# Optimization experiments

Hardware: AMD Instinct MI355X
Metric: run time of the kernel (lower is better)

## Reference

```python
import jax, jax.numpy as jnp
import numpy as np

STRIDE = 16
NUM_A = 9
POS_TH, NEG_TH = 0.7, 0.3
FG, BG, IGN = 1.0, 0.0, 2.0
CAP = 128  # BATCH_SIZE * 0.5 for both fg and bg


def _generate_base_anchors(base_size=16, ratios=(0.5, 1.0, 2.0), scales=(8, 16, 32)):
    w = h = float(base_size)
    xc = yc = 0.5 * (base_size - 1)
    size = w * h
    out = []
    for r in ratios:
        ws = np.round(np.sqrt(size / r))
        hs = np.round(ws * r)
        for s in scales:
            W, H = ws * s, hs * s
            out.append([xc - 0.5 * (W - 1), yc - 0.5 * (H - 1),
                        xc + 0.5 * (W - 1), yc + 0.5 * (H - 1)])
    return np.asarray(out, dtype=np.float32)  # [9,4]


def _all_anchors(H, W):
    base = _generate_base_anchors()
    sx = np.arange(W, dtype=np.float32) * STRIDE
    sy = np.arange(H, dtype=np.float32) * STRIDE
    xs, ys = np.meshgrid(sx, sy)  # row-major over (h, w)
    shifts = np.stack([xs.ravel(), ys.ravel(), xs.ravel(), ys.ravel()], 1)
    return jnp.asarray((shifts[:, None, :] + base[None, :, :]).reshape(-1, 4))  # [H*W*9,4], order (h,w,a)


def _forward(scores, gt, im_w, im_h):
    H, W = scores.shape[2], scores.shape[3]
    anchors = _all_anchors(H, W)  # [N,4]
    valid = (anchors[:, 0] >= 0.) & (anchors[:, 1] >= 0.) & \
            (anchors[:, 2] < im_w) & (anchors[:, 3] < im_h)
    # pairwise IoU with +1 box convention
    aw = anchors[:, 2] - anchors[:, 0] + 1.
    ah = anchors[:, 3] - anchors[:, 1] + 1.
    a_area = jnp.where((aw > 0) & (ah > 0), aw * ah, 0.)
    gw = gt[:, 2] - gt[:, 0] + 1.
    gh = gt[:, 3] - gt[:, 1] + 1.
    g_area = jnp.where((gw > 0) & (gh > 0), gw * gh, 0.)
    ix1 = jnp.maximum(anchors[:, None, 0], gt[None, :, 0])
    iy1 = jnp.maximum(anchors[:, None, 1], gt[None, :, 1])
    ix2 = jnp.minimum(anchors[:, None, 2], gt[None, :, 2])
    iy2 = jnp.minimum(anchors[:, None, 3], gt[None, :, 3])
    iw = ix2 - ix1 + 1.
    ih = iy2 - iy1 + 1.
    inter = jnp.where((iw > 0) & (ih > 0), iw * ih, 0.)
    ovl = inter / (a_area[:, None] + g_area[None, :] - inter)  # [N,G]
    ovl_m = jnp.where(valid[:, None], ovl, -1.)  # exclude invalid anchors
    a_argmax = jnp.argmax(ovl, axis=1)           # best gt per anchor
    a_max = jnp.max(ovl, axis=1)
    g_max = jnp.max(ovl_m, axis=0)               # best (valid) anchor overlap per gt
    gt_fg = jnp.any(ovl_m == g_max[None, :], axis=1) & valid
    labels = jnp.where(valid & (a_max < NEG_TH), BG, IGN)
    labels = jnp.where(gt_fg, FG, labels)
    labels = jnp.where(valid & (a_max >= POS_TH), FG, labels)
    # random subsample fg/bg down to CAP each (matches npr.choice semantics in distribution)
    kf, kb = jax.random.split(jax.random.key(42))
    def subsample(lbl, mask, k):
        s = jnp.where(mask, jax.random.uniform(k, lbl.shape), jnp.inf)
        ranks = jnp.argsort(jnp.argsort(s))
        keep = ranks < jnp.minimum(jnp.sum(mask), CAP)
        return jnp.where(mask & ~keep, IGN, lbl)
    labels = subsample(labels, labels == FG, kf)
    labels = subsample(labels, labels == BG, kb)
    num_ni = jnp.sum(labels != IGN).astype(jnp.float32)
    gts = gt[a_argmax]
    ax = (anchors[:, 2] + anchors[:, 0]) * 0.5
    ay = (anchors[:, 3] + anchors[:, 1]) * 0.5
    gwm = gts[:, 2] - gts[:, 0] + 1.
    ghm = gts[:, 3] - gts[:, 1] + 1.
    gx = (gts[:, 2] + gts[:, 0]) * 0.5
    gy = (gts[:, 3] + gts[:, 1]) * 0.5
    adj = jnp.stack([(gx - ax) / aw, (gy - ay) / ah,
                     jnp.log(gwm / aw), jnp.log(ghm / ah)], axis=1)  # [N,4]
    adj = jnp.where(valid[:, None], adj, 0.)
    wts = jnp.where((labels == FG)[:, None], 1.0 / num_ni, 0.) * jnp.ones((1, 4), jnp.float32)
    labels_out = labels.reshape(1, H, W, NUM_A).transpose(0, 3, 1, 2) \
                       .reshape(1, 1, NUM_A * H, W).astype(jnp.int32)
    adj_out = adj.reshape(1, H, W, 4 * NUM_A).transpose(0, 3, 1, 2)
    wts_out = wts.reshape(1, H, W, 4 * NUM_A).transpose(0, 3, 1, 2)
    return labels_out, adj_out, wts_out


def setup_inputs() -> dict:
    key = jax.random.key(0)
    k1, k2, k3 = jax.random.split(key, 3)
    scores = jax.random.normal(k1, (1, 18, 256, 256), dtype=jnp.float32)
    G = 64
    cxy = jax.random.uniform(k2, (G, 2), minval=100., maxval=3900.)
    wh = jax.random.uniform(k3, (G, 2), minval=32., maxval=512.)
    x1y1 = jnp.clip(cxy - wh * 0.5, 0., 4095.)
    x2y2 = jnp.clip(cxy + wh * 0.5, 0., 4095.)
    gt = jnp.concatenate([x1y1, x2y2], axis=1)  # [G,4] = x1,y1,x2,y2
    return {"anchor_object_scores": scores, "ground_truth_boxes": gt,
            "im_w": 4096, "im_h": 4096}


def reference(anchor_object_scores, ground_truth_boxes, im_w, im_h):
    return _forward(anchor_object_scores, ground_truth_boxes, im_w, im_h)
```

## Files before the change

### kernel.cpp

```cpp
#include <hip/hip_runtime.h>
#include <stdint.h>


#define NUM_A 9
#define HW 65536
#define N_ANCH 589824
#define NG 64
#define CAPK 128u
#define NBIN 2048
#define BIN_SHIFT 12
#define CAND_CAP 4096

#define LAB_BG 0u
#define LAB_FG 1u
#define LAB_IGN 2u

#define OFF_GMAX8 0
#define OFF_HF    512
#define OFF_HB    (OFF_HF + NBIN)
#define OFF_CNTF  (OFF_HF + 2*NBIN)
#define OFF_CNTB  (OFF_CNTF + 1)
#define OFF_DONE2 (OFF_CNTF + 2)
#define OFF_SEL   (OFF_CNTF + 4)
#define OFF_CANDF 4620
#define OFF_CANDB (OFF_CANDF + 2*CAND_CAP)
#define OFF_LABM  (OFF_CANDB + 2*CAND_CAP)
#define ZERO_BEG  OFF_HF
#define ZERO_END  OFF_CANDF
#define NZ        (ZERO_END - ZERO_BEG)

__constant__ float BA[NUM_A][4] = {
  { -84.f,  -40.f,  99.f,  55.f}, {-176.f,  -88.f, 191.f, 103.f},
  {-360.f, -184.f, 375.f, 199.f}, { -56.f,  -56.f,  71.f,  71.f},
  {-120.f, -120.f, 135.f, 135.f}, {-248.f, -248.f, 263.f, 263.f},
  { -36.f,  -80.f,  51.f,  95.f}, { -80.f, -168.f,  95.f, 183.f},
  {-168.f, -344.f, 183.f, 359.f}};

__host__ __device__ static inline void tf2x32(uint32_t k0, uint32_t k1,
                                              uint32_t x0, uint32_t x1,
                                              uint32_t* o0, uint32_t* o1) {
  const uint32_t ks2 = k0 ^ k1 ^ 0x1BD11BDAu;
#define TF_R(r) { x0 += x1; x1 = (x1 << (r)) | (x1 >> (32 - (r))); x1 ^= x0; }
  x0 += k0; x1 += k1;
  TF_R(13) TF_R(15) TF_R(26) TF_R(6)
  x0 += k1;  x1 += ks2 + 1u;
  TF_R(17) TF_R(29) TF_R(16) TF_R(24)
  x0 += ks2; x1 += k0 + 2u;
  TF_R(13) TF_R(15) TF_R(26) TF_R(6)
  x0 += k0;  x1 += k1 + 3u;
  TF_R(17) TF_R(29) TF_R(16) TF_R(24)
  x0 += k1;  x1 += ks2 + 4u;
  TF_R(13) TF_R(15) TF_R(26) TF_R(6)
  x0 += ks2; x1 += k0 + 5u;
#undef TF_R
  *o0 = x0; *o1 = x1;
}

__device__ static inline uint32_t mant_of(uint32_t k0, uint32_t k1, uint32_t n) {
  uint32_t o0, o1;
  tf2x32(k0, k1, 0u, n, &o0, &o1);
  return (o0 ^ o1) >> 9;
}

__device__ static inline float iou1(float a0, float a1, float a2, float a3,
                                    float aarea, float g0, float g1, float g2,
                                    float g3, float garea) {
  #pragma clang fp contract(off)
  float ix1 = fmaxf(a0, g0);
  float iy1 = fmaxf(a1, g1);
  float ix2 = fminf(a2, g2);
  float iy2 = fminf(a3, g3);
  float iw = ix2 - ix1 + 1.0f;
  float ih = iy2 - iy1 + 1.0f;
  float inter = (iw > 0.0f && ih > 0.0f) ? iw * ih : 0.0f;
  float den = aarea + garea - inter;
  return inter / den;
}

__global__ __launch_bounds__(256) void k_gmax(const float* __restrict__ gt,
                                              const int* __restrict__ imw_p,
                                              const int* __restrict__ imh_p,
                                              uint32_t* __restrict__ ws) {
  #pragma clang fp contract(off)
  int tid = threadIdx.x;
  int b = blockIdx.x;
  int gid = b * 256 + tid;
  if (gid < NZ) ws[ZERO_BEG + gid] = 0u;

  int g = b >> 3, sl = b & 7;
  float g0 = gt[g*4+0], g1 = gt[g*4+1], g2 = gt[g*4+2], g3 = gt[g*4+3];
  float gw = g2 - g0 + 1.0f, gh = g3 - g1 + 1.0f;
  float ga = (gw > 0.0f && gh > 0.0f) ? gw * gh : 0.0f;
  float imw = (float)imw_p[0], imh = (float)imh_p[0];

  float mx = 0.0f;
  for (int a = 0; a < NUM_A; a++) {
    float b0 = BA[a][0], b1 = BA[a][1], b2 = BA[a][2], b3 = BA[a][3];
    int wlo = max(0,   (int)floorf((g0 - 1.0f - b2) * 0.0625f));
    int whi = min(255, (int)ceilf ((g2 + 1.0f - b0) * 0.0625f));
    int hlo = max(0,   (int)floorf((g1 - 1.0f - b3) * 0.0625f));
    int hhi = min(255, (int)ceilf ((g3 + 1.0f - b1) * 0.0625f));
    int wx = whi - wlo + 1, wy = hhi - hlo + 1;
    if (wx <= 0 || wy <= 0) continue;
    int tot = wx * wy;
    for (int idx = sl * 256 + tid; idx < tot; idx += 2048) {
      int h = hlo + idx / wx, w = wlo + idx % wx;
      float sx = (float)(w << 4), sy = (float)(h << 4);
      float x1 = b0 + sx, y1 = b1 + sy, x2 = b2 + sx, y2 = b3 + sy;
      float aw = x2 - x1 + 1.0f, ah = y2 - y1 + 1.0f;
      float aarea = aw * ah;
      bool vld = (x1 >= 0.0f) && (y1 >= 0.0f) && (x2 < imw) && (y2 < imh);
      float o = iou1(x1, y1, x2, y2, aarea, g0, g1, g2, g3, ga);
      if (vld) mx = fmaxf(mx, o);
    }
  }
  #pragma unroll
  for (int s = 32; s >= 1; s >>= 1) mx = fmaxf(mx, __shfl_xor(mx, s, 64));
  __shared__ float wmax[4];
  if ((tid & 63) == 0) wmax[tid >> 6] = mx;
  __syncthreads();
  if (tid == 0) {
    float m = fmaxf(fmaxf(wmax[0], wmax[1]), fmaxf(wmax[2], wmax[3]));
    ws[OFF_GMAX8 + g * 8 + sl] = __float_as_uint(m);
  }
}

__global__ __launch_bounds__(256) void k_main(const float* __restrict__ gt,
                                              const int* __restrict__ imw_p,
                                              const int* __restrict__ imh_p,
                                              float* __restrict__ out_adj,
                                              uint32_t* __restrict__ ws,
                                              uint32_t kf0, uint32_t kf1,
                                              uint32_t kb0, uint32_t kb1) {
  #pragma clang fp contract(off)
  __shared__ float sg0[NG], sg1[NG], sg2[NG], sg3[NG], sga[NG], sgm[NG];
  __shared__ uint32_t sh[2 * NBIN];
  __shared__ unsigned long long sMask[4];
  __shared__ int sAnyZero, sLast;
  int tid = threadIdx.x;
  {
    uint4* sh4 = (uint4*)sh;
    #pragma unroll
    for (int k = 0; k < 4; k++) sh4[tid + k * 256] = make_uint4(0, 0, 0, 0);
  }
  if (tid == 0) sAnyZero = 0;
  if (tid < NG) {
    const float4 g4 = ((const float4*)gt)[tid];
    sg0[tid] = g4.x; sg1[tid] = g4.y; sg2[tid] = g4.z; sg3[tid] = g4.w;
    float gw = g4.z - g4.x + 1.0f, gh = g4.w - g4.y + 1.0f;
    sga[tid] = (gw > 0.0f && gh > 0.0f) ? gw * gh : 0.0f;
    uint32_t mm = 0u;
    #pragma unroll
    for (int j = 0; j < 8; j++) mm = max(mm, ws[OFF_GMAX8 + tid * 8 + j]);
    sgm[tid] = __uint_as_float(mm);
    if (mm == 0u) atomicOr(&sAnyZero, 1);
  }
  __syncthreads();

  int b = blockIdx.x;
  int a = b >> 6, hb = (b & 63) << 2;
  float BA0 = BA[a][0], BA1 = BA[a][1], BA2 = BA[a][2], BA3 = BA[a][3];

  {
    int wv = tid >> 6, g = tid & 63;
    float sy = (float)((hb + wv) << 4);
    float ihp = fminf(BA3 + sy, sg3[g]) - fmaxf(BA1 + sy, sg1[g]) + 1.0f;
    unsigned long long mk = __ballot(ihp > 0.0f);
    if (g == 0) sMask[wv] = mk;
  }
  __syncthreads();

  float imw = (float)imw_p[0], imh = (float)imh_p[0];
  int w = tid;
  float sx = (float)(w << 4);
  float A0 = BA0 + sx, A2 = BA2 + sx;
  float aw = A2 - A0 + 1.0f;
  float A1v[4], A3v[4];
  #pragma unroll
  for (int r = 0; r < 4; r++) {
    float sy = (float)((hb + r) << 4);
    A1v[r] = BA1 + sy; A3v[r] = BA3 + sy;
  }
  float ah = A3v[0] - A1v[0] + 1.0f;
  float aarea = aw * ah;
  bool xv = (A0 >= 0.0f) && (A2 < imw);

  unsigned long long mk0 = sMask[0], mk1 = sMask[1],
                     mk2 = sMask[2], mk3 = sMask[3];
  unsigned long long uni = mk0 | mk1 | mk2 | mk3;
  float amaxv[4] = {0.f, 0.f, 0.f, 0.f};
  int bgv[4] = {0, 0, 0, 0};
  uint32_t afv = 0u;
  while (uni) {
    int g = __ffsll(uni) - 1;
    uni &= uni - 1;
    float iw = fminf(A2, sg2[g]) - fmaxf(A0, sg0[g]) + 1.0f;
    if (!__any(iw > 0.0f)) continue;
    if (iw > 0.0f) {
      float base = aarea + sga[g];
      float gy1 = sg1[g], gy2 = sg3[g], gm = sgm[g];
#define DO_ROW(r, mk)                                                     \
      if ((mk >> g) & 1ull) {                                             \
        float ih = fminf(A3v[r], gy2) - fmaxf(A1v[r], gy1) + 1.0f;        \
        float inter = iw * ih;                                            \
        float o = inter / (base - inter);                                 \
        if (o > amaxv[r]) { amaxv[r] = o; bgv[r] = g; }                   \
        if (o == gm) afv |= (1u << r);                                    \
      }
      DO_ROW(0, mk0) DO_ROW(1, mk1) DO_ROW(2, mk2) DO_ROW(3, mk3)
#undef DO_ROW
    }
  }

  bool anyZ = (sAnyZero != 0);
  #pragma unroll
  for (int r = 0; r < 4; r++) {
    int hw = (hb + r) * 256 + w;
    bool valid = xv && (A1v[r] >= 0.0f) && (A3v[r] < imh);
    float amax = amaxv[r];
    bool anyfg = (((afv >> r) & 1u) || anyZ) && valid;
    uint32_t lab;
    if (!valid)                       lab = LAB_IGN;
    else if (anyfg || amax >= 0.7f)   lab = LAB_FG;
    else if (amax < 0.3f)             lab = LAB_BG;
    else                              lab = LAB_IGN;

    float adj0 = 0.f, adj1 = 0.f, adj2 = 0.f, adj3 = 0.f;
    if (valid) {
      int bg = bgv[r];
      float G0 = sg0[bg], G1 = sg1[bg], G2 = sg2[bg], G3 = sg3[bg];
      float ax = (A2 + A0) * 0.5f, ay = (A3v[r] + A1v[r]) * 0.5f;
      float gwm = G2 - G0 + 1.0f, ghm = G3 - G1 + 1.0f;
      float gx = (G2 + G0) * 0.5f, gy = (G3 + G1) * 0.5f;
      adj0 = (gx - ax) / aw;
      adj1 = (gy - ay) / ah;
      adj2 = logf(gwm / aw);
      adj3 = logf(ghm / ah);
    }
    int c4 = a * 4;
    out_adj[(c4 + 0) * HW + hw] = adj0;
    out_adj[(c4 + 1) * HW + hw] = adj1;
    out_adj[(c4 + 2) * HW + hw] = adj2;
    out_adj[(c4 + 3) * HW + hw] = adj3;

    uint32_t m = 0u;
    uint32_t n = (uint32_t)(hw * 9 + a);
    if (lab != LAB_IGN) {
      uint32_t kk0 = (lab == LAB_FG) ? kf0 : kb0;
      uint32_t kk1 = (lab == LAB_FG) ? kf1 : kb1;
      m = mant_of(kk0, kk1, n);
      atomicAdd(&sh[((lab == LAB_FG) ? 0 : NBIN) + (m >> BIN_SHIFT)], 1u);
    }
    ws[OFF_LABM + a * HW + hw] = (lab << 24) | m;
  }

  __syncthreads();
  for (int i = tid; i < 2 * NBIN; i += 256) {
    uint32_t v = sh[i];
    if (v) atomicAdd(&ws[OFF_HF + i], v);
  }
  __syncthreads();
  if (tid == 0)
    sLast = (atomicAdd(&ws[OFF_DONE2], 1u) == 575u) ? 1 : 0;
  __syncthreads();
  if (sLast) {
    for (int cls = 0; cls < 2; cls++) {
      uint32_t* hist = ws + (cls ? OFF_HB : OFF_HF);
      uint32_t* sel = ws + OFF_SEL + cls * 4;
      uint32_t loc[8], s = 0;
      #pragma unroll
      for (int j = 0; j < 8; j++) {
        loc[j] = __hip_atomic_load(&hist[tid * 8 + j], __ATOMIC_RELAXED,
                                   __HIP_MEMORY_SCOPE_AGENT);
        s += loc[j];
      }
      sh[tid] = s; __syncthreads();
      for (int off = 1; off < 256; off <<= 1) {
        uint32_t v = (tid >= off) ? sh[tid - off] : 0u;
        __syncthreads();
        sh[tid] += v;
        __syncthreads();
      }
      uint32_t total = sh[255];
      uint32_t K = total < CAPK ? total : CAPK;
      if (tid == 0) {
        sel[3] = K;
        if (K == 0u) { sel[0] = 0xFFFFFFFFu; sel[1] = 0u; sel[2] = 0u; }
      }
      if (K > 0u) {
        uint32_t myC = sh[tid], pvC = (tid == 0) ? 0u : sh[tid - 1];
        if (myC >= K && pvC < K) {
          uint32_t cum = pvC; int bb = tid * 8;
          for (int j = 0; j < 8; j++) {
            if (cum + loc[j] >= K) { bb = tid * 8 + j; break; }
            cum += loc[j];
          }
          sel[0] = (uint32_t)bb; sel[1] = cum; sel[2] = K - cum;
        }
      }
      __syncthreads();
    }
  }
}

__global__ __launch_bounds__(256) void k_emit(float* __restrict__ out_lab,
                                              float* __restrict__ out_wts,
                                              uint32_t* __restrict__ ws) {
  int t = blockIdx.x * 256 + threadIdx.x;
  uint32_t lm = ws[OFF_LABM + t];
  uint32_t lab = lm >> 24;
  uint32_t m = lm & 0x7FFFFFu;
  uint32_t Kf = ws[OFF_SEL + 3], Kb = ws[OFF_SEL + 7];
  float inv = 1.0f / (float)(Kf + Kb);
  int a = t >> 16, hw = t & 65535;
  uint32_t n = (uint32_t)(hw * 9 + a);

  float outv = 2.0f, wv = 0.0f;
  if (lab == LAB_FG) {
    uint32_t b = m >> BIN_SHIFT, bf = ws[OFF_SEL + 0];
    if (b < bf) { outv = 1.0f; wv = inv; }
    else if (b == bf) {
      uint32_t idx = atomicAdd(&ws[OFF_CNTF], 1u);
      if (idx < CAND_CAP)
        ((uint64_t*)(ws + OFF_CANDF))[idx] = ((uint64_t)m << 20) | (uint64_t)n;
    }
  } else if (lab == LAB_BG) {
    uint32_t b = m >> BIN_SHIFT, bb = ws[OFF_SEL + 4];
    if (b < bb) { outv = 0.0f; }
    else if (b == bb) {
      uint32_t idx = atomicAdd(&ws[OFF_CNTB], 1u);
      if (idx < CAND_CAP)
        ((uint64_t*)(ws + OFF_CANDB))[idx] = ((uint64_t)m << 20) | (uint64_t)n;
    }
  }
  out_lab[t] = outv;
  int c4 = a * 4;
  out_wts[(c4 + 0) * HW + hw] = wv;
  out_wts[(c4 + 1) * HW + hw] = wv;
  out_wts[(c4 + 2) * HW + hw] = wv;
  out_wts[(c4 + 3) * HW + hw] = wv;
}

__global__ __launch_bounds__(256) void k_fixup(float* __restrict__ out_lab,
                                               float* __restrict__ out_wts,
                                               uint32_t* __restrict__ ws) {
  __shared__ uint64_t sc[CAND_CAP];
  int cls = blockIdx.x;
  uint32_t cnt = ws[cls == 0 ? OFF_CNTF : OFF_CNTB];
  uint32_t C = cnt < CAND_CAP ? cnt : CAND_CAP;
  uint32_t need = ws[OFF_SEL + cls * 4 + 2];
  uint32_t Kf = ws[OFF_SEL + 3], Kb = ws[OFF_SEL + 7];
  float inv = 1.0f / (float)(Kf + Kb);
  const uint64_t* cand =
      (const uint64_t*)(ws + (cls == 0 ? OFF_CANDF : OFF_CANDB));
  for (uint32_t i = threadIdx.x; i < C; i += 256) sc[i] = cand[i];
  __syncthreads();
  for (uint32_t i = threadIdx.x; i < C; i += 256) {
    uint64_t k = sc[i];
    uint32_t r = 0;
    for (uint32_t j = 0; j < C; j++) r += (sc[j] < k) ? 1u : 0u;
    if (r < need) {
      uint32_t n = (uint32_t)(k & 0xFFFFFu);
      uint32_t a = n % 9u, hw = n / 9u;
      uint32_t t = a * HW + hw;
      if (cls == 0) {
        out_lab[t] = 1.0f;
        #pragma unroll
        for (int j = 0; j < 4; j++) out_wts[(a * 4 + j) * HW + hw] = inv;
      } else {
        out_lab[t] = 0.0f;
      }
    }
  }
}

extern "C" void kernel_launch(void* const* d_in, const int* in_sizes, int n_in,
                              void* d_out, int out_size, void* d_ws,
                              size_t ws_size, hipStream_t stream) {
  const float* gt  = (const float*)d_in[1];
  const int*   imw = (const int*)d_in[2];
  const int*   imh = (const int*)d_in[3];
  float* out      = (float*)d_out;
  float* out_lab  = out;
  float* out_adj  = out + N_ANCH;
  float* out_wts  = out + 5 * N_ANCH;
  uint32_t* ws = (uint32_t*)d_ws;

  uint32_t kf0, kf1, kb0, kb1;
  tf2x32(0u, 42u, 0u, 0u, &kf0, &kf1);
  tf2x32(0u, 42u, 0u, 1u, &kb0, &kb1);

  hipLaunchKernelGGL(k_gmax, dim3(NG * 8), dim3(256), 0, stream, gt, imw, imh,
                     ws);
  hipLaunchKernelGGL(k_main, dim3(576), dim3(256), 0, stream, gt, imw, imh,
                     out_adj, ws, kf0, kf1, kb0, kb1);
  hipLaunchKernelGGL(k_emit, dim3(N_ANCH / 256), dim3(256), 0, stream, out_lab,
                     out_wts, ws);
  hipLaunchKernelGGL(k_fixup, dim3(2), dim3(256), 0, stream, out_lab, out_wts,
                     ws);
}
```

Measured before the change: 101.9 us.

## Fuse four kernels into one cooperative kernel with grid syncs

Merges the gt-max, main IoU/label, emit and fixup kernels into a single cooperative launch of 576 blocks separated by grid-wide barriers. Labels and random mantissas are kept in registers across the barrier instead of being written to and reread from workspace. The gt-max phase is spread over all 576 blocks (9 per gt) instead of 512. This removes three kernel launch gaps and a workspace round trip, but adds grid-sync costs and depends on all 576 blocks being co-resident. If the cooperative launch fails, it falls back to the old four-kernel path.

```diff
diff --git a/kernel.cpp b/kernel.cpp
--- a/kernel.cpp
+++ b/kernel.cpp
@@ -1,5 +1,8 @@
 #include <hip/hip_runtime.h>
+#include <hip/hip_cooperative_groups.h>
 #include <stdint.h>
+
+namespace cg = cooperative_groups;
 
 
 #define NUM_A 9
@@ -14,6 +17,18 @@
 #define LAB_BG 0u
 #define LAB_FG 1u
 #define LAB_IGN 2u
+
+#define F_OFF_GMAX 0
+#define F_OFF_HF   1024
+#define F_OFF_HB   (F_OFF_HF + NBIN)
+#define F_OFF_CNTF (F_OFF_HF + 2*NBIN)
+#define F_OFF_CNTB (F_OFF_CNTF + 1)
+#define F_OFF_DONE (F_OFF_CNTF + 2)
+#define F_OFF_SEL  (F_OFF_CNTF + 4)
+#define F_OFF_CANDF 5132
+#define F_OFF_CANDB (F_OFF_CANDF + 2*CAND_CAP)
+#define F_ZERO_BEG F_OFF_HF
+#define F_NZ (F_OFF_CANDF - F_OFF_HF)
 
 #define OFF_GMAX8 0
 #define OFF_HF    512
@@ -77,73 +92,81 @@
   return inter / den;
 }
 
-__global__ __launch_bounds__(256) void k_gmax(const float* __restrict__ gt,
-                                              const int* __restrict__ imw_p,
-                                              const int* __restrict__ imh_p,
-                                              uint32_t* __restrict__ ws) {
+__global__ __launch_bounds__(256, 3) void k_fused(
+    const float* __restrict__ gt, const int* __restrict__ imw_p,
+    const int* __restrict__ imh_p, float* __restrict__ out_lab,
+    float* __restrict__ out_adj, float* __restrict__ out_wts,
+    uint32_t* __restrict__ ws, uint32_t kf0, uint32_t kf1, uint32_t kb0,
+    uint32_t kb1) {
   #pragma clang fp contract(off)
+  cg::grid_group grd = cg::this_grid();
+
+  __shared__ uint64_t SMEM[CAND_CAP];
+  uint32_t* SW = (uint32_t*)SMEM;
+  float* sg0 = (float*)(SW + 0);
+  float* sg1 = (float*)(SW + 64);
+  float* sg2 = (float*)(SW + 128);
+  float* sg3 = (float*)(SW + 192);
+  float* sga = (float*)(SW + 256);
+  float* sgm = (float*)(SW + 320);
+  uint32_t* sh = SW + 384;
+  unsigned long long* sMask = (unsigned long long*)(SW + 4480);
+  int* sAnyZero = (int*)(SW + 4488);
+  int* sLast = (int*)(SW + 4489);
+  float* wmax = (float*)(SW + 4490);
+
   int tid = threadIdx.x;
   int b = blockIdx.x;
-  int gid = b * 256 + tid;
-  if (gid < NZ) ws[ZERO_BEG + gid] = 0u;
-
-  int g = b >> 3, sl = b & 7;
-  float g0 = gt[g*4+0], g1 = gt[g*4+1], g2 = gt[g*4+2], g3 = gt[g*4+3];
-  float gw = g2 - g0 + 1.0f, gh = g3 - g1 + 1.0f;
-  float ga = (gw > 0.0f && gh > 0.0f) ? gw * gh : 0.0f;
-  float imw = (float)imw_p[0], imh = (float)imh_p[0];
-
-  float mx = 0.0f;
-  for (int a = 0; a < NUM_A; a++) {
-    float b0 = BA[a][0], b1 = BA[a][1], b2 = BA[a][2], b3 = BA[a][3];
-    int wlo = max(0,   (int)floorf((g0 - 1.0f - b2) * 0.0625f));
-    int whi = min(255, (int)ceilf ((g2 + 1.0f - b0) * 0.0625f));
-    int hlo = max(0,   (int)floorf((g1 - 1.0f - b3) * 0.0625f));
-    int hhi = min(255, (int)ceilf ((g3 + 1.0f - b1) * 0.0625f));
-    int wx = whi - wlo + 1, wy = hhi - hlo + 1;
-    if (wx <= 0 || wy <= 0) continue;
-    int tot = wx * wy;
-    for (int idx = sl * 256 + tid; idx < tot; idx += 2048) {
-      int h = hlo + idx / wx, w = wlo + idx % wx;
-      float sx = (float)(w << 4), sy = (float)(h << 4);
-      float x1 = b0 + sx, y1 = b1 + sy, x2 = b2 + sx, y2 = b3 + sy;
-      float aw = x2 - x1 + 1.0f, ah = y2 - y1 + 1.0f;
-      float aarea = aw * ah;
-      bool vld = (x1 >= 0.0f) && (y1 >= 0.0f) && (x2 < imw) && (y2 < imh);
-      float o = iou1(x1, y1, x2, y2, aarea, g0, g1, g2, g3, ga);
-      if (vld) mx = fmaxf(mx, o);
-    }
-  }
-  #pragma unroll
-  for (int s = 32; s >= 1; s >>= 1) mx = fmaxf(mx, __shfl_xor(mx, s, 64));
-  __shared__ float wmax[4];
-  if ((tid & 63) == 0) wmax[tid >> 6] = mx;
-  __syncthreads();
-  if (tid == 0) {
-    float m = fmaxf(fmaxf(wmax[0], wmax[1]), fmaxf(wmax[2], wmax[3]));
-    ws[OFF_GMAX8 + g * 8 + sl] = __float_as_uint(m);
-  }
-}
-
-__global__ __launch_bounds__(256) void k_main(const float* __restrict__ gt,
-                                              const int* __restrict__ imw_p,
-                                              const int* __restrict__ imh_p,
-                                              float* __restrict__ out_adj,
-                                              uint32_t* __restrict__ ws,
-                                              uint32_t kf0, uint32_t kf1,
-                                              uint32_t kb0, uint32_t kb1) {
-  #pragma clang fp contract(off)
-  __shared__ float sg0[NG], sg1[NG], sg2[NG], sg3[NG], sga[NG], sgm[NG];
-  __shared__ uint32_t sh[2 * NBIN];
-  __shared__ unsigned long long sMask[4];
-  __shared__ int sAnyZero, sLast;
-  int tid = threadIdx.x;
+
+  {
+    int gid = b * 256 + tid;
+    if (gid < F_NZ) ws[F_ZERO_BEG + gid] = 0u;
+
+    int g = b / 9, sl = b - g * 9;
+    float g0 = gt[g*4+0], g1 = gt[g*4+1], g2 = gt[g*4+2], g3 = gt[g*4+3];
+    float gw = g2 - g0 + 1.0f, gh = g3 - g1 + 1.0f;
+    float ga = (gw > 0.0f && gh > 0.0f) ? gw * gh : 0.0f;
+    float imw = (float)imw_p[0], imh = (float)imh_p[0];
+
+    float mx = 0.0f;
+    for (int aa = 0; aa < NUM_A; aa++) {
+      float b0 = BA[aa][0], b1 = BA[aa][1], b2 = BA[aa][2], b3 = BA[aa][3];
+      int wlo = max(0,   (int)floorf((g0 - 1.0f - b2) * 0.0625f));
+      int whi = min(255, (int)ceilf ((g2 + 1.0f - b0) * 0.0625f));
+      int hlo = max(0,   (int)floorf((g1 - 1.0f - b3) * 0.0625f));
+      int hhi = min(255, (int)ceilf ((g3 + 1.0f - b1) * 0.0625f));
+      int wx = whi - wlo + 1, wy = hhi - hlo + 1;
+      if (wx <= 0 || wy <= 0) continue;
+      int tot = wx * wy;
+      for (int idx = sl * 256 + tid; idx < tot; idx += 2304) {
+        int h = hlo + idx / wx, w2 = wlo + idx % wx;
+        float sx = (float)(w2 << 4), sy = (float)(h << 4);
+        float x1 = b0 + sx, y1 = b1 + sy, x2 = b2 + sx, y2 = b3 + sy;
+        float aw = x2 - x1 + 1.0f, ah = y2 - y1 + 1.0f;
+        float aarea = aw * ah;
+        bool vld = (x1 >= 0.0f) && (y1 >= 0.0f) && (x2 < imw) && (y2 < imh);
+        float o = iou1(x1, y1, x2, y2, aarea, g0, g1, g2, g3, ga);
+        if (vld) mx = fmaxf(mx, o);
+      }
+    }
+    #pragma unroll
+    for (int s = 32; s >= 1; s >>= 1) mx = fmaxf(mx, __shfl_xor(mx, s, 64));
+    if ((tid & 63) == 0) wmax[tid >> 6] = mx;
+    __syncthreads();
+    if (tid == 0) {
+      float m = fmaxf(fmaxf(wmax[0], wmax[1]), fmaxf(wmax[2], wmax[3]));
+      ws[F_OFF_GMAX + g * 16 + sl] = __float_as_uint(m);
+    }
+  }
+
+  grd.sync();
+
   {
     uint4* sh4 = (uint4*)sh;
     #pragma unroll
     for (int k = 0; k < 4; k++) sh4[tid + k * 256] = make_uint4(0, 0, 0, 0);
   }
-  if (tid == 0) sAnyZero = 0;
+  if (tid == 0) *sAnyZero = 0;
   if (tid < NG) {
     const float4 g4 = ((const float4*)gt)[tid];
     sg0[tid] = g4.x; sg1[tid] = g4.y; sg2[tid] = g4.z; sg3[tid] = g4.w;
@@ -151,13 +174,15 @@
     sga[tid] = (gw > 0.0f && gh > 0.0f) ? gw * gh : 0.0f;
     uint32_t mm = 0u;
     #pragma unroll
-    for (int j = 0; j < 8; j++) mm = max(mm, ws[OFF_GMAX8 + tid * 8 + j]);
+    for (int j = 0; j < 9; j++)
+      mm = max(mm, __hip_atomic_load(&ws[F_OFF_GMAX + tid * 16 + j],
+                                     __ATOMIC_RELAXED,
+                                     __HIP_MEMORY_SCOPE_AGENT));
     sgm[tid] = __uint_as_float(mm);
-    if (mm == 0u) atomicOr(&sAnyZero, 1);
-  }
-  __syncthreads();
-
-  int b = blockIdx.x;
+    if (mm == 0u) atomicOr(sAnyZero, 1);
+  }
+  __syncthreads();
+
   int a = b >> 6, hb = (b & 63) << 2;
   float BA0 = BA[a][0], BA1 = BA[a][1], BA2 = BA[a][2], BA3 = BA[a][3];
 
@@ -212,6 +237,315 @@
     }
   }
 
+  bool anyZ = (*sAnyZero != 0);
+  uint32_t lm[4];
+  #pragma unroll
+  for (int r = 0; r < 4; r++) {
+    int hw = (hb + r) * 256 + w;
+    bool valid = xv && (A1v[r] >= 0.0f) && (A3v[r] < imh);
+    float amax = amaxv[r];
+    bool anyfg = (((afv >> r) & 1u) || anyZ) && valid;
+    uint32_t lab;
+    if (!valid)                       lab = LAB_IGN;
+    else if (anyfg || amax >= 0.7f)   lab = LAB_FG;
+    else if (amax < 0.3f)             lab = LAB_BG;
+    else                              lab = LAB_IGN;
+
+    float adj0 = 0.f, adj1 = 0.f, adj2 = 0.f, adj3 = 0.f;
+    if (valid) {
+      int bg = bgv[r];
+      float G0 = sg0[bg], G1 = sg1[bg], G2 = sg2[bg], G3 = sg3[bg];
+      float ax = (A2 + A0) * 0.5f, ay = (A3v[r] + A1v[r]) * 0.5f;
+      float gwm = G2 - G0 + 1.0f, ghm = G3 - G1 + 1.0f;
+      float gx = (G2 + G0) * 0.5f, gy = (G3 + G1) * 0.5f;
+      adj0 = (gx - ax) / aw;
+      adj1 = (gy - ay) / ah;
+      adj2 = logf(gwm / aw);
+      adj3 = logf(ghm / ah);
+    }
+    int c4 = a * 4;
+    out_adj[(c4 + 0) * HW + hw] = adj0;
+    out_adj[(c4 + 1) * HW + hw] = adj1;
+    out_adj[(c4 + 2) * HW + hw] = adj2;
+    out_adj[(c4 + 3) * HW + hw] = adj3;
+
+    uint32_t m = 0u;
+    uint32_t n = (uint32_t)(hw * 9 + a);
+    if (lab != LAB_IGN) {
+      uint32_t kk0 = (lab == LAB_FG) ? kf0 : kb0;
+      uint32_t kk1 = (lab == LAB_FG) ? kf1 : kb1;
+      m = mant_of(kk0, kk1, n);
+      atomicAdd(&sh[((lab == LAB_FG) ? 0 : NBIN) + (m >> BIN_SHIFT)], 1u);
+    }
+    lm[r] = (lab << 24) | m;
+  }
+
+  __syncthreads();
+  for (int i = tid; i < 2 * NBIN; i += 256) {
+    uint32_t v = sh[i];
+    if (v) atomicAdd(&ws[F_OFF_HF + i], v);
+  }
+  __syncthreads();
+  if (tid == 0)
+    *sLast = (atomicAdd(&ws[F_OFF_DONE], 1u) == 575u) ? 1 : 0;
+  __syncthreads();
+  if (*sLast) {
+    for (int cls = 0; cls < 2; cls++) {
+      uint32_t* hist = ws + (cls ? F_OFF_HB : F_OFF_HF);
+      uint32_t* sel = ws + F_OFF_SEL + cls * 4;
+      uint32_t loc[8], s = 0;
+      #pragma unroll
+      for (int j = 0; j < 8; j++) {
+        loc[j] = __hip_atomic_load(&hist[tid * 8 + j], __ATOMIC_RELAXED,
+                                   __HIP_MEMORY_SCOPE_AGENT);
+        s += loc[j];
+      }
+      sh[tid] = s; __syncthreads();
+      for (int off = 1; off < 256; off <<= 1) {
+        uint32_t v = (tid >= off) ? sh[tid - off] : 0u;
+        __syncthreads();
+        sh[tid] += v;
+        __syncthreads();
+      }
+      uint32_t total = sh[255];
+      uint32_t K = total < CAPK ? total : CAPK;
+      if (tid == 0) {
+        sel[3] = K;
+        if (K == 0u) { sel[0] = 0xFFFFFFFFu; sel[1] = 0u; sel[2] = 0u; }
+      }
+      if (K > 0u) {
+        uint32_t myC = sh[tid], pvC = (tid == 0) ? 0u : sh[tid - 1];
+        if (myC >= K && pvC < K) {
+          uint32_t cum = pvC; int bb = tid * 8;
+          for (int j = 0; j < 8; j++) {
+            if (cum + loc[j] >= K) { bb = tid * 8 + j; break; }
+            cum += loc[j];
+          }
+          sel[0] = (uint32_t)bb; sel[1] = cum; sel[2] = K - cum;
+        }
+      }
+      __syncthreads();
+    }
+  }
+
+  grd.sync();
+
+  uint32_t bf = __hip_atomic_load(&ws[F_OFF_SEL + 0], __ATOMIC_RELAXED,
+                                  __HIP_MEMORY_SCOPE_AGENT);
+  uint32_t Kf = __hip_atomic_load(&ws[F_OFF_SEL + 3], __ATOMIC_RELAXED,
+                                  __HIP_MEMORY_SCOPE_AGENT);
+  uint32_t bbnd = __hip_atomic_load(&ws[F_OFF_SEL + 4], __ATOMIC_RELAXED,
+                                    __HIP_MEMORY_SCOPE_AGENT);
+  uint32_t Kb = __hip_atomic_load(&ws[F_OFF_SEL + 7], __ATOMIC_RELAXED,
+                                  __HIP_MEMORY_SCOPE_AGENT);
+  float inv = 1.0f / (float)(Kf + Kb);
+  #pragma unroll
+  for (int r = 0; r < 4; r++) {
+    int hw = (hb + r) * 256 + w;
+    uint32_t lab = lm[r] >> 24;
+    uint32_t m = lm[r] & 0x7FFFFFu;
+    uint32_t n = (uint32_t)(hw * 9 + a);
+    float outv = 2.0f, wv = 0.0f;
+    if (lab == LAB_FG) {
+      uint32_t bn = m >> BIN_SHIFT;
+      if (bn < bf) { outv = 1.0f; wv = inv; }
+      else if (bn == bf) {
+        uint32_t idx = atomicAdd(&ws[F_OFF_CNTF], 1u);
+        if (idx < CAND_CAP)
+          ((uint64_t*)(ws + F_OFF_CANDF))[idx] =
+              ((uint64_t)m << 20) | (uint64_t)n;
+      }
+    } else if (lab == LAB_BG) {
+      uint32_t bn = m >> BIN_SHIFT;
+      if (bn < bbnd) { outv = 0.0f; }
+      else if (bn == bbnd) {
+        uint32_t idx = atomicAdd(&ws[F_OFF_CNTB], 1u);
+        if (idx < CAND_CAP)
+          ((uint64_t*)(ws + F_OFF_CANDB))[idx] =
+              ((uint64_t)m << 20) | (uint64_t)n;
+      }
+    }
+    out_lab[a * HW + hw] = outv;
+    int c4 = a * 4;
+    out_wts[(c4 + 0) * HW + hw] = wv;
+    out_wts[(c4 + 1) * HW + hw] = wv;
+    out_wts[(c4 + 2) * HW + hw] = wv;
+    out_wts[(c4 + 3) * HW + hw] = wv;
+  }
+
+  grd.sync();
+
+  if (b < 2) {
+    int cls = b;
+    uint32_t cnt = __hip_atomic_load(
+        &ws[cls == 0 ? F_OFF_CNTF : F_OFF_CNTB], __ATOMIC_RELAXED,
+        __HIP_MEMORY_SCOPE_AGENT);
+    uint32_t C = cnt < CAND_CAP ? cnt : CAND_CAP;
+    uint32_t need = __hip_atomic_load(&ws[F_OFF_SEL + cls * 4 + 2],
+                                      __ATOMIC_RELAXED,
+                                      __HIP_MEMORY_SCOPE_AGENT);
+    const uint64_t* cand =
+        (const uint64_t*)(ws + (cls == 0 ? F_OFF_CANDF : F_OFF_CANDB));
+    for (uint32_t i = tid; i < C; i += 256)
+      SMEM[i] = __hip_atomic_load(&cand[i], __ATOMIC_RELAXED,
+                                  __HIP_MEMORY_SCOPE_AGENT);
+    __syncthreads();
+    for (uint32_t i = tid; i < C; i += 256) {
+      uint64_t k = SMEM[i];
+      uint32_t rr = 0;
+      for (uint32_t j = 0; j < C; j++) rr += (SMEM[j] < k) ? 1u : 0u;
+      if (rr < need) {
+        uint32_t n = (uint32_t)(k & 0xFFFFFu);
+        uint32_t aa = n % 9u, hww = n / 9u;
+        uint32_t t = aa * HW + hww;
+        if (cls == 0) {
+          out_lab[t] = 1.0f;
+          #pragma unroll
+          for (int j2 = 0; j2 < 4; j2++)
+            out_wts[(aa * 4 + j2) * HW + hww] = inv;
+        } else {
+          out_lab[t] = 0.0f;
+        }
+      }
+    }
+  }
+}
+
+__global__ __launch_bounds__(256) void k_gmax(const float* __restrict__ gt,
+                                              const int* __restrict__ imw_p,
+                                              const int* __restrict__ imh_p,
+                                              uint32_t* __restrict__ ws) {
+  #pragma clang fp contract(off)
+  int tid = threadIdx.x;
+  int b = blockIdx.x;
+  int gid = b * 256 + tid;
+  if (gid < NZ) ws[ZERO_BEG + gid] = 0u;
+
+  int g = b >> 3, sl = b & 7;
+  float g0 = gt[g*4+0], g1 = gt[g*4+1], g2 = gt[g*4+2], g3 = gt[g*4+3];
+  float gw = g2 - g0 + 1.0f, gh = g3 - g1 + 1.0f;
+  float ga = (gw > 0.0f && gh > 0.0f) ? gw * gh : 0.0f;
+  float imw = (float)imw_p[0], imh = (float)imh_p[0];
+
+  float mx = 0.0f;
+  for (int a = 0; a < NUM_A; a++) {
+    float b0 = BA[a][0], b1 = BA[a][1], b2 = BA[a][2], b3 = BA[a][3];
+    int wlo = max(0,   (int)floorf((g0 - 1.0f - b2) * 0.0625f));
+    int whi = min(255, (int)ceilf ((g2 + 1.0f - b0) * 0.0625f));
+    int hlo = max(0,   (int)floorf((g1 - 1.0f - b3) * 0.0625f));
+    int hhi = min(255, (int)ceilf ((g3 + 1.0f - b1) * 0.0625f));
+    int wx = whi - wlo + 1, wy = hhi - hlo + 1;
+    if (wx <= 0 || wy <= 0) continue;
+    int tot = wx * wy;
+    for (int idx = sl * 256 + tid; idx < tot; idx += 2048) {
+      int h = hlo + idx / wx, w = wlo + idx % wx;
+      float sx = (float)(w << 4), sy = (float)(h << 4);
+      float x1 = b0 + sx, y1 = b1 + sy, x2 = b2 + sx, y2 = b3 + sy;
+      float aw = x2 - x1 + 1.0f, ah = y2 - y1 + 1.0f;
+      float aarea = aw * ah;
+      bool vld = (x1 >= 0.0f) && (y1 >= 0.0f) && (x2 < imw) && (y2 < imh);
+      float o = iou1(x1, y1, x2, y2, aarea, g0, g1, g2, g3, ga);
+      if (vld) mx = fmaxf(mx, o);
+    }
+  }
+  #pragma unroll
+  for (int s = 32; s >= 1; s >>= 1) mx = fmaxf(mx, __shfl_xor(mx, s, 64));
+  __shared__ float wmax[4];
+  if ((tid & 63) == 0) wmax[tid >> 6] = mx;
+  __syncthreads();
+  if (tid == 0) {
+    float m = fmaxf(fmaxf(wmax[0], wmax[1]), fmaxf(wmax[2], wmax[3]));
+    ws[OFF_GMAX8 + g * 8 + sl] = __float_as_uint(m);
+  }
+}
+
+__global__ __launch_bounds__(256) void k_main(const float* __restrict__ gt,
+                                              const int* __restrict__ imw_p,
+                                              const int* __restrict__ imh_p,
+                                              float* __restrict__ out_adj,
+                                              uint32_t* __restrict__ ws,
+                                              uint32_t kf0, uint32_t kf1,
+                                              uint32_t kb0, uint32_t kb1) {
+  #pragma clang fp contract(off)
+  __shared__ float sg0[NG], sg1[NG], sg2[NG], sg3[NG], sga[NG], sgm[NG];
+  __shared__ uint32_t sh[2 * NBIN];
+  __shared__ unsigned long long sMask[4];
+  __shared__ int sAnyZero, sLast;
+  int tid = threadIdx.x;
+  {
+    uint4* sh4 = (uint4*)sh;
+    #pragma unroll
+    for (int k = 0; k < 4; k++) sh4[tid + k * 256] = make_uint4(0, 0, 0, 0);
+  }
+  if (tid == 0) sAnyZero = 0;
+  if (tid < NG) {
+    const float4 g4 = ((const float4*)gt)[tid];
+    sg0[tid] = g4.x; sg1[tid] = g4.y; sg2[tid] = g4.z; sg3[tid] = g4.w;
+    float gw = g4.z - g4.x + 1.0f, gh = g4.w - g4.y + 1.0f;
+    sga[tid] = (gw > 0.0f && gh > 0.0f) ? gw * gh : 0.0f;
+    uint32_t mm = 0u;
+    #pragma unroll
+    for (int j = 0; j < 8; j++) mm = max(mm, ws[OFF_GMAX8 + tid * 8 + j]);
+    sgm[tid] = __uint_as_float(mm);
+    if (mm == 0u) atomicOr(&sAnyZero, 1);
+  }
+  __syncthreads();
+
+  int b = blockIdx.x;
+  int a = b >> 6, hb = (b & 63) << 2;
+  float BA0 = BA[a][0], BA1 = BA[a][1], BA2 = BA[a][2], BA3 = BA[a][3];
+
+  {
+    int wv = tid >> 6, g = tid & 63;
+    float sy = (float)((hb + wv) << 4);
+    float ihp = fminf(BA3 + sy, sg3[g]) - fmaxf(BA1 + sy, sg1[g]) + 1.0f;
+    unsigned long long mk = __ballot(ihp > 0.0f);
+    if (g == 0) sMask[wv] = mk;
+  }
+  __syncthreads();
+
+  float imw = (float)imw_p[0], imh = (float)imh_p[0];
+  int w = tid;
+  float sx = (float)(w << 4);
+  float A0 = BA0 + sx, A2 = BA2 + sx;
+  float aw = A2 - A0 + 1.0f;
+  float A1v[4], A3v[4];
+  #pragma unroll
+  for (int r = 0; r < 4; r++) {
+    float sy = (float)((hb + r) << 4);
+    A1v[r] = BA1 + sy; A3v[r] = BA3 + sy;
+  }
+  float ah = A3v[0] - A1v[0] + 1.0f;
+  float aarea = aw * ah;
+  bool xv = (A0 >= 0.0f) && (A2 < imw);
+
+  unsigned long long mk0 = sMask[0], mk1 = sMask[1],
+                     mk2 = sMask[2], mk3 = sMask[3];
+  unsigned long long uni = mk0 | mk1 | mk2 | mk3;
+  float amaxv[4] = {0.f, 0.f, 0.f, 0.f};
+  int bgv[4] = {0, 0, 0, 0};
+  uint32_t afv = 0u;
+  while (uni) {
+    int g = __ffsll(uni) - 1;
+    uni &= uni - 1;
+    float iw = fminf(A2, sg2[g]) - fmaxf(A0, sg0[g]) + 1.0f;
+    if (!__any(iw > 0.0f)) continue;
+    if (iw > 0.0f) {
+      float base = aarea + sga[g];
+      float gy1 = sg1[g], gy2 = sg3[g], gm = sgm[g];
+#define DO_ROW(r, mk)                                                     \
+      if ((mk >> g) & 1ull) {                                             \
+        float ih = fminf(A3v[r], gy2) - fmaxf(A1v[r], gy1) + 1.0f;        \
+        float inter = iw * ih;                                            \
+        float o = inter / (base - inter);                                 \
+        if (o > amaxv[r]) { amaxv[r] = o; bgv[r] = g; }                   \
+        if (o == gm) afv |= (1u << r);                                    \
+      }
+      DO_ROW(0, mk0) DO_ROW(1, mk1) DO_ROW(2, mk2) DO_ROW(3, mk3)
+#undef DO_ROW
+    }
+  }
+
   bool anyZ = (sAnyZero != 0);
   #pragma unroll
   for (int r = 0; r < 4; r++) {
@@ -390,12 +724,21 @@
   tf2x32(0u, 42u, 0u, 0u, &kf0, &kf1);
   tf2x32(0u, 42u, 0u, 1u, &kb0, &kb1);
 
-  hipLaunchKernelGGL(k_gmax, dim3(NG * 8), dim3(256), 0, stream, gt, imw, imh,
-                     ws);
-  hipLaunchKernelGGL(k_main, dim3(576), dim3(256), 0, stream, gt, imw, imh,
-                     out_adj, ws, kf0, kf1, kb0, kb1);
-  hipLaunchKernelGGL(k_emit, dim3(N_ANCH / 256), dim3(256), 0, stream, out_lab,
-                     out_wts, ws);
-  hipLaunchKernelGGL(k_fixup, dim3(2), dim3(256), 0, stream, out_lab, out_wts,
-                     ws);
-}
+  void* kargs[] = {(void*)&gt,      (void*)&imw,     (void*)&imh,
+                   (void*)&out_lab, (void*)&out_adj, (void*)&out_wts,
+                   (void*)&ws,      (void*)&kf0,     (void*)&kf1,
+                   (void*)&kb0,     (void*)&kb1};
+  hipError_t err = hipLaunchCooperativeKernel(
+      (const void*)k_fused, dim3(576), dim3(256), kargs, 0, stream);
+  if (err != hipSuccess) {
+    (void)hipGetLastError();
+    hipLaunchKernelGGL(k_gmax, dim3(NG * 8), dim3(256), 0, stream, gt, imw,
+                       imh, ws);
+    hipLaunchKernelGGL(k_main, dim3(576), dim3(256), 0, stream, gt, imw, imh,
+                       out_adj, ws, kf0, kf1, kb0, kb1);
+    hipLaunchKernelGGL(k_emit, dim3(N_ANCH / 256), dim3(256), 0, stream,
+                       out_lab, out_wts, ws);
+    hipLaunchKernelGGL(k_fixup, dim3(2), dim3(256), 0, stream, out_lab,
+                       out_wts, ws);
+  }
+}
```

Measured after the change: 308.3 us. 203% more time.

## Compute per-GT max IoU analytically per block and fuse fixup into emit kernel

Applied to the files above, without the earlier changes.

Drops the brute-force k_gmax kernel, which scanned every overlapping anchor per ground-truth box. Each main block now derives the best IoU per (gt, anchor shape) analytically by testing a few candidate shifts per axis, taking the max into shared memory. The tie-break fixup kernel is folded into the emit kernel through a last-block-done counter, and workspace zeroing moves to a memset. Together these remove two launches and the scan work, but every block repeats the gt-max computation, and the analytic candidate search must match the exhaustive max exactly.

```diff
diff --git a/kernel.cpp b/kernel.cpp
--- a/kernel.cpp
+++ b/kernel.cpp
@@ -15,19 +15,20 @@
 #define LAB_FG 1u
 #define LAB_IGN 2u
 
-#define OFF_GMAX8 0
-#define OFF_HF    512
-#define OFF_HB    (OFF_HF + NBIN)
-#define OFF_CNTF  (OFF_HF + 2*NBIN)
+#define OFF_HF    0
+#define OFF_HB    NBIN
+#define OFF_CNTF  (2*NBIN)
 #define OFF_CNTB  (OFF_CNTF + 1)
-#define OFF_DONE2 (OFF_CNTF + 2)
+#define OFF_DONE  (OFF_CNTF + 2)
+#define OFF_DONE2 (OFF_CNTF + 3)
 #define OFF_SEL   (OFF_CNTF + 4)
-#define OFF_CANDF 4620
+#define CTRL_WORDS 4108
+#define OFF_CANDF 4108
 #define OFF_CANDB (OFF_CANDF + 2*CAND_CAP)
 #define OFF_LABM  (OFF_CANDB + 2*CAND_CAP)
-#define ZERO_BEG  OFF_HF
-#define ZERO_END  OFF_CANDF
-#define NZ        (ZERO_END - ZERO_BEG)
+
+#define NBLK_MAIN 576
+#define NBLK_EMIT (N_ANCH / 256)
 
 __constant__ float BA[NUM_A][4] = {
   { -84.f,  -40.f,  99.f,  55.f}, {-176.f,  -88.f, 191.f, 103.f},
@@ -62,82 +63,45 @@
   return (o0 ^ o1) >> 9;
 }
 
-__device__ static inline float iou1(float a0, float a1, float a2, float a3,
-                                    float aarea, float g0, float g1, float g2,
-                                    float g3, float garea) {
+__device__ static inline float axis_best(float blo, float bhi, float glo,
+                                         float ghi, int lo, int hi) {
   #pragma clang fp contract(off)
-  float ix1 = fmaxf(a0, g0);
-  float iy1 = fmaxf(a1, g1);
-  float ix2 = fminf(a2, g2);
-  float iy2 = fminf(a3, g3);
-  float iw = ix2 - ix1 + 1.0f;
-  float ih = iy2 - iy1 + 1.0f;
-  float inter = (iw > 0.0f && ih > 0.0f) ? iw * ih : 0.0f;
-  float den = aarea + garea - inter;
-  return inter / den;
-}
-
-__global__ __launch_bounds__(256) void k_gmax(const float* __restrict__ gt,
-                                              const int* __restrict__ imw_p,
-                                              const int* __restrict__ imh_p,
-                                              uint32_t* __restrict__ ws) {
-  #pragma clang fp contract(off)
-  int tid = threadIdx.x;
-  int b = blockIdx.x;
-  int gid = b * 256 + tid;
-  if (gid < NZ) ws[ZERO_BEG + gid] = 0u;
-
-  int g = b >> 3, sl = b & 7;
-  float g0 = gt[g*4+0], g1 = gt[g*4+1], g2 = gt[g*4+2], g3 = gt[g*4+3];
-  float gw = g2 - g0 + 1.0f, gh = g3 - g1 + 1.0f;
-  float ga = (gw > 0.0f && gh > 0.0f) ? gw * gh : 0.0f;
-  float imw = (float)imw_p[0], imh = (float)imh_p[0];
-
-  float mx = 0.0f;
-  for (int a = 0; a < NUM_A; a++) {
-    float b0 = BA[a][0], b1 = BA[a][1], b2 = BA[a][2], b3 = BA[a][3];
-    int wlo = max(0,   (int)floorf((g0 - 1.0f - b2) * 0.0625f));
-    int whi = min(255, (int)ceilf ((g2 + 1.0f - b0) * 0.0625f));
-    int hlo = max(0,   (int)floorf((g1 - 1.0f - b3) * 0.0625f));
-    int hhi = min(255, (int)ceilf ((g3 + 1.0f - b1) * 0.0625f));
-    int wx = whi - wlo + 1, wy = hhi - hlo + 1;
-    if (wx <= 0 || wy <= 0) continue;
-    int tot = wx * wy;
-    for (int idx = sl * 256 + tid; idx < tot; idx += 2048) {
-      int h = hlo + idx / wx, w = wlo + idx % wx;
-      float sx = (float)(w << 4), sy = (float)(h << 4);
-      float x1 = b0 + sx, y1 = b1 + sy, x2 = b2 + sx, y2 = b3 + sy;
-      float aw = x2 - x1 + 1.0f, ah = y2 - y1 + 1.0f;
-      float aarea = aw * ah;
-      bool vld = (x1 >= 0.0f) && (y1 >= 0.0f) && (x2 < imw) && (y2 < imh);
-      float o = iou1(x1, y1, x2, y2, aarea, g0, g1, g2, g3, ga);
-      if (vld) mx = fmaxf(mx, o);
-    }
-  }
+  float t1 = (ghi - bhi) * 0.0625f;
+  float t2 = (glo - blo) * 0.0625f;
+  float tmin = fminf(t1, t2), tmax = fmaxf(t1, t2);
+  int c1 = (int)floorf(tmin), c2 = (int)ceilf(tmax);
+  int cand0 = lo, cand1 = hi;
+  int cand2 = min(max(c1,     lo), hi);
+  int cand3 = min(max(c1 + 1, lo), hi);
+  int cand4 = min(max(c2 - 1, lo), hi);
+  int cand5 = min(max(c2,     lo), hi);
+  float best = -3.0e38f;
+  int cands[6] = {cand0, cand1, cand2, cand3, cand4, cand5};
   #pragma unroll
-  for (int s = 32; s >= 1; s >>= 1) mx = fmaxf(mx, __shfl_xor(mx, s, 64));
-  __shared__ float wmax[4];
-  if ((tid & 63) == 0) wmax[tid >> 6] = mx;
-  __syncthreads();
-  if (tid == 0) {
-    float m = fmaxf(fmaxf(wmax[0], wmax[1]), fmaxf(wmax[2], wmax[3]));
-    ws[OFF_GMAX8 + g * 8 + sl] = __float_as_uint(m);
-  }
-}
-
-__global__ __launch_bounds__(256) void k_main(const float* __restrict__ gt,
-                                              const int* __restrict__ imw_p,
-                                              const int* __restrict__ imh_p,
-                                              float* __restrict__ out_adj,
-                                              uint32_t* __restrict__ ws,
-                                              uint32_t kf0, uint32_t kf1,
-                                              uint32_t kb0, uint32_t kb1) {
+  for (int i = 0; i < 6; i++) {
+    float s = (float)(cands[i] << 4);
+    float v = fminf(bhi + s, ghi) - fmaxf(blo + s, glo) + 1.0f;
+    best = fmaxf(best, v);
+  }
+  return best;
+}
+
+__global__ __launch_bounds__(256) void k_main2(const float* __restrict__ gt,
+                                               const int* __restrict__ imw_p,
+                                               const int* __restrict__ imh_p,
+                                               float* __restrict__ out_adj,
+                                               uint32_t* __restrict__ ws,
+                                               uint32_t kf0, uint32_t kf1,
+                                               uint32_t kb0, uint32_t kb1) {
   #pragma clang fp contract(off)
   __shared__ float sg0[NG], sg1[NG], sg2[NG], sg3[NG], sga[NG], sgm[NG];
+  __shared__ uint32_t sgmU[NG];
   __shared__ uint32_t sh[2 * NBIN];
   __shared__ unsigned long long sMask[4];
   __shared__ int sAnyZero, sLast;
   int tid = threadIdx.x;
+  int b = blockIdx.x;
+  int a = b >> 6, hb = (b & 63) << 2;
   {
     uint4* sh4 = (uint4*)sh;
     #pragma unroll
@@ -149,27 +113,48 @@
     sg0[tid] = g4.x; sg1[tid] = g4.y; sg2[tid] = g4.z; sg3[tid] = g4.w;
     float gw = g4.z - g4.x + 1.0f, gh = g4.w - g4.y + 1.0f;
     sga[tid] = (gw > 0.0f && gh > 0.0f) ? gw * gh : 0.0f;
-    uint32_t mm = 0u;
-    #pragma unroll
-    for (int j = 0; j < 8; j++) mm = max(mm, ws[OFF_GMAX8 + tid * 8 + j]);
-    sgm[tid] = __uint_as_float(mm);
-    if (mm == 0u) atomicOr(&sAnyZero, 1);
-  }
-  __syncthreads();
-
-  int b = blockIdx.x;
-  int a = b >> 6, hb = (b & 63) << 2;
-  float BA0 = BA[a][0], BA1 = BA[a][1], BA2 = BA[a][2], BA3 = BA[a][3];
+    sgmU[tid] = 0u;
+  }
+  __syncthreads();
+
+  {
+    int imwi = imw_p[0], imhi = imh_p[0];
+    for (int p = tid; p < NG * NUM_A; p += 256) {
+      int g = p / NUM_A, q = p - g * NUM_A;
+      float b0 = BA[q][0], b1 = BA[q][1], b2 = BA[q][2], b3 = BA[q][3];
+      int ib0 = (int)b0, ib1 = (int)b1, ib2 = (int)b2, ib3 = (int)b3;
+      int wlo = max(0, (-ib0 + 15) >> 4);
+      int whi = min(255, (imwi - ib2 - 1) >> 4);
+      int hlo = max(0, (-ib1 + 15) >> 4);
+      int hhi = min(255, (imhi - ib3 - 1) >> 4);
+      if (wlo > whi || hlo > hhi) continue;
+      float iwb = axis_best(b0, b2, sg0[g], sg2[g], wlo, whi);
+      float ihb = axis_best(b1, b3, sg1[g], sg3[g], hlo, hhi);
+      float aw = b2 - b0 + 1.0f, ah = b3 - b1 + 1.0f;
+      float aarea = aw * ah;
+      float inter = (iwb > 0.0f && ihb > 0.0f) ? iwb * ihb : 0.0f;
+      float den = aarea + sga[g] - inter;
+      float o = inter / den;
+      atomicMax(&sgmU[g], __float_as_uint(o));
+    }
+  }
 
   {
     int wv = tid >> 6, g = tid & 63;
     float sy = (float)((hb + wv) << 4);
-    float ihp = fminf(BA3 + sy, sg3[g]) - fmaxf(BA1 + sy, sg1[g]) + 1.0f;
+    float ihp = fminf(BA[a][3] + sy, sg3[g]) - fmaxf(BA[a][1] + sy, sg1[g]) + 1.0f;
     unsigned long long mk = __ballot(ihp > 0.0f);
     if (g == 0) sMask[wv] = mk;
   }
   __syncthreads();
-
+  if (tid < NG) {
+    uint32_t mm = sgmU[tid];
+    sgm[tid] = __uint_as_float(mm);
+    if (mm == 0u) atomicOr(&sAnyZero, 1);
+  }
+  __syncthreads();
+
+  float BA0 = BA[a][0], BA1 = BA[a][1], BA2 = BA[a][2], BA3 = BA[a][3];
   float imw = (float)imw_p[0], imh = (float)imh_p[0];
   int w = tid;
   float sx = (float)(w << 4);
@@ -261,7 +246,7 @@
   }
   __syncthreads();
   if (tid == 0)
-    sLast = (atomicAdd(&ws[OFF_DONE2], 1u) == 575u) ? 1 : 0;
+    sLast = (atomicAdd(&ws[OFF_DONE], 1u) == NBLK_MAIN - 1) ? 1 : 0;
   __syncthreads();
   if (sLast) {
     for (int cls = 0; cls < 2; cls++) {
@@ -303,10 +288,13 @@
   }
 }
 
-__global__ __launch_bounds__(256) void k_emit(float* __restrict__ out_lab,
-                                              float* __restrict__ out_wts,
-                                              uint32_t* __restrict__ ws) {
-  int t = blockIdx.x * 256 + threadIdx.x;
+__global__ __launch_bounds__(256) void k_emit2(float* __restrict__ out_lab,
+                                               float* __restrict__ out_wts,
+                                               uint32_t* __restrict__ ws) {
+  __shared__ uint64_t sc[CAND_CAP];
+  __shared__ int sLast;
+  int tid = threadIdx.x;
+  int t = blockIdx.x * 256 + tid;
   uint32_t lm = ws[OFF_LABM + t];
   uint32_t lab = lm >> 24;
   uint32_t m = lm & 0x7FFFFFu;
@@ -317,20 +305,24 @@
 
   float outv = 2.0f, wv = 0.0f;
   if (lab == LAB_FG) {
-    uint32_t b = m >> BIN_SHIFT, bf = ws[OFF_SEL + 0];
-    if (b < bf) { outv = 1.0f; wv = inv; }
-    else if (b == bf) {
+    uint32_t bn = m >> BIN_SHIFT, bf = ws[OFF_SEL + 0];
+    if (bn < bf) { outv = 1.0f; wv = inv; }
+    else if (bn == bf) {
       uint32_t idx = atomicAdd(&ws[OFF_CNTF], 1u);
       if (idx < CAND_CAP)
-        ((uint64_t*)(ws + OFF_CANDF))[idx] = ((uint64_t)m << 20) | (uint64_t)n;
+        __hip_atomic_store((uint64_t*)(ws + OFF_CANDF) + idx,
+                           ((uint64_t)m << 20) | (uint64_t)n,
+                           __ATOMIC_RELAXED, __HIP_MEMORY_SCOPE_AGENT);
     }
   } else if (lab == LAB_BG) {
-    uint32_t b = m >> BIN_SHIFT, bb = ws[OFF_SEL + 4];
-    if (b < bb) { outv = 0.0f; }
-    else if (b == bb) {
+    uint32_t bn = m >> BIN_SHIFT, bb = ws[OFF_SEL + 4];
+    if (bn < bb) { outv = 0.0f; }
+    else if (bn == bb) {
       uint32_t idx = atomicAdd(&ws[OFF_CNTB], 1u);
       if (idx < CAND_CAP)
-        ((uint64_t*)(ws + OFF_CANDB))[idx] = ((uint64_t)m << 20) | (uint64_t)n;
+        __hip_atomic_store((uint64_t*)(ws + OFF_CANDB) + idx,
+                           ((uint64_t)m << 20) | (uint64_t)n,
+                           __ATOMIC_RELAXED, __HIP_MEMORY_SCOPE_AGENT);
     }
   }
   out_lab[t] = outv;
@@ -339,37 +331,45 @@
   out_wts[(c4 + 1) * HW + hw] = wv;
   out_wts[(c4 + 2) * HW + hw] = wv;
   out_wts[(c4 + 3) * HW + hw] = wv;
-}
-
-__global__ __launch_bounds__(256) void k_fixup(float* __restrict__ out_lab,
-                                               float* __restrict__ out_wts,
-                                               uint32_t* __restrict__ ws) {
-  __shared__ uint64_t sc[CAND_CAP];
-  int cls = blockIdx.x;
-  uint32_t cnt = ws[cls == 0 ? OFF_CNTF : OFF_CNTB];
-  uint32_t C = cnt < CAND_CAP ? cnt : CAND_CAP;
-  uint32_t need = ws[OFF_SEL + cls * 4 + 2];
-  uint32_t Kf = ws[OFF_SEL + 3], Kb = ws[OFF_SEL + 7];
-  float inv = 1.0f / (float)(Kf + Kb);
-  const uint64_t* cand =
-      (const uint64_t*)(ws + (cls == 0 ? OFF_CANDF : OFF_CANDB));
-  for (uint32_t i = threadIdx.x; i < C; i += 256) sc[i] = cand[i];
-  __syncthreads();
-  for (uint32_t i = threadIdx.x; i < C; i += 256) {
-    uint64_t k = sc[i];
-    uint32_t r = 0;
-    for (uint32_t j = 0; j < C; j++) r += (sc[j] < k) ? 1u : 0u;
-    if (r < need) {
-      uint32_t n = (uint32_t)(k & 0xFFFFFu);
-      uint32_t a = n % 9u, hw = n / 9u;
-      uint32_t t = a * HW + hw;
-      if (cls == 0) {
-        out_lab[t] = 1.0f;
-        #pragma unroll
-        for (int j = 0; j < 4; j++) out_wts[(a * 4 + j) * HW + hw] = inv;
-      } else {
-        out_lab[t] = 0.0f;
-      }
+
+  __syncthreads();
+  if (tid == 0)
+    sLast = (__hip_atomic_fetch_add(&ws[OFF_DONE2], 1u, __ATOMIC_ACQ_REL,
+                                    __HIP_MEMORY_SCOPE_AGENT)
+             == NBLK_EMIT - 1) ? 1 : 0;
+  __syncthreads();
+  if (sLast) {
+    for (int cls = 0; cls < 2; cls++) {
+      uint32_t cnt = __hip_atomic_load(&ws[cls == 0 ? OFF_CNTF : OFF_CNTB],
+                                       __ATOMIC_RELAXED,
+                                       __HIP_MEMORY_SCOPE_AGENT);
+      uint32_t C = cnt < CAND_CAP ? cnt : CAND_CAP;
+      uint32_t need = ws[OFF_SEL + cls * 4 + 2];
+      const uint64_t* cand =
+          (const uint64_t*)(ws + (cls == 0 ? OFF_CANDF : OFF_CANDB));
+      for (uint32_t i = tid; i < C; i += 256)
+        sc[i] = __hip_atomic_load(&cand[i], __ATOMIC_RELAXED,
+                                  __HIP_MEMORY_SCOPE_AGENT);
+      __syncthreads();
+      for (uint32_t i = tid; i < C; i += 256) {
+        uint64_t k = sc[i];
+        uint32_t rr = 0;
+        for (uint32_t j = 0; j < C; j++) rr += (sc[j] < k) ? 1u : 0u;
+        if (rr < need) {
+          uint32_t nn = (uint32_t)(k & 0xFFFFFu);
+          uint32_t aa = nn % 9u, hww = nn / 9u;
+          uint32_t tt = aa * HW + hww;
+          if (cls == 0) {
+            out_lab[tt] = 1.0f;
+            #pragma unroll
+            for (int j2 = 0; j2 < 4; j2++)
+              out_wts[(aa * 4 + j2) * HW + hww] = inv;
+          } else {
+            out_lab[tt] = 0.0f;
+          }
+        }
+      }
+      __syncthreads();
     }
   }
 }
@@ -390,12 +390,9 @@
   tf2x32(0u, 42u, 0u, 0u, &kf0, &kf1);
   tf2x32(0u, 42u, 0u, 1u, &kb0, &kb1);
 
-  hipLaunchKernelGGL(k_gmax, dim3(NG * 8), dim3(256), 0, stream, gt, imw, imh,
-                     ws);
-  hipLaunchKernelGGL(k_main, dim3(576), dim3(256), 0, stream, gt, imw, imh,
-                     out_adj, ws, kf0, kf1, kb0, kb1);
-  hipLaunchKernelGGL(k_emit, dim3(N_ANCH / 256), dim3(256), 0, stream, out_lab,
+  hipMemsetAsync(ws, 0, CTRL_WORDS * sizeof(uint32_t), stream);
+  hipLaunchKernelGGL(k_main2, dim3(NBLK_MAIN), dim3(256), 0, stream, gt, imw,
+                     imh, out_adj, ws, kf0, kf1, kb0, kb1);
+  hipLaunchKernelGGL(k_emit2, dim3(NBLK_EMIT), dim3(256), 0, stream, out_lab,
                      out_wts, ws);
-  hipLaunchKernelGGL(k_fixup, dim3(2), dim3(256), 0, stream, out_lab, out_wts,
-                     ws);
-}
+}
```

Measured after the change: 156.6 us. 1.54x slower.
